# Optimization experiments

Hardware: AMD Instinct MI355X
Metric: run time of the kernel (lower is better)

The kernel has to match this reference:

```python
import jax, jax.numpy as jnp
import numpy as np

N, E = 50000, 1600000
D_IN, D_OUT = 256, 64
ALPHA = 0.2        # LeakyReLU slope used on attention logits (self.leakyrelu)
BT_SLOPE = 0.01    # F.leaky_relu default slope inside relu_bt


def _xavier_normal(key, shape, gain):
    fan_in, fan_out = shape[0], shape[1]
    std = gain * np.sqrt(2.0 / (fan_in + fan_out))
    return jax.random.normal(key, shape, dtype=jnp.float32) * std


def relu_bt(x):
    # -threshold(-leaky_relu(x), -t, -t) == min(leaky_relu(x), t), t = ||x||_inf (detached)
    t = jax.lax.stop_gradient(jnp.max(jnp.abs(x)))
    y = jnp.where(x >= 0, x, BT_SLOPE * x)
    return jnp.minimum(y, t)


def setup_inputs() -> dict:
    key = jax.random.key(0)
    k0, k1, k2, k3, k4, k5 = jax.random.split(key, 6)
    inp = jax.random.normal(k0, (N, D_IN), dtype=jnp.float32)
    edge = jax.random.randint(k1, (2, E), 0, N, dtype=jnp.int64)
    W_high = _xavier_normal(k2, (D_IN, D_OUT), 1.414)
    W_low = _xavier_normal(k3, (D_IN, D_OUT), 1.414)
    a_high = _xavier_normal(k4, (1, D_OUT), 1.414)
    a_low = _xavier_normal(k5, (1, D_OUT), 1.414)
    return {"input": inp, "edge": edge, "W_high": W_high, "W_low": W_low,
            "a_high": a_high, "a_low": a_low}


def reference(input, edge, W_high, W_low, a_high, a_low):
    n = input.shape[0]
    src, dst = edge[0], edge[1]

    h_high = relu_bt(input @ W_high)  # [N, D_OUT]
    h_low = relu_bt(input @ W_low)    # [N, D_OUT]

    # a @ (h[src] -/+ h[dst])^T == (a.h)[src] -/+ (a.h)[dst]: compute per-node scalar
    # projections first, then gather scalars per edge (avoids [E, D_OUT] edge features).
    s_high = h_high @ a_high[0]       # [N]
    s_low = h_low @ a_low[0]          # [N]

    def lrelu(x):
        return jnp.where(x >= 0, x, ALPHA * x)

    edge_e_high = jnp.exp(-lrelu(s_high[src] - s_high[dst]))  # [E]
    edge_e_low = jnp.exp(-lrelu(s_low[src] + s_low[dst]))     # [E]
    # dropout p=0.0 -> identity

    # sparse A @ ones -> per-row sum of attention weights
    rowsum_high = jax.ops.segment_sum(edge_e_high, src, num_segments=n)[:, None]
    rowsum_low = jax.ops.segment_sum(edge_e_low, src, num_segments=n)[:, None]

    # sparse A @ h -> weighted aggregation of neighbor features
    hp_high = jax.ops.segment_sum(edge_e_high[:, None] * h_high[dst], src, num_segments=n)
    hp_low = jax.ops.segment_sum(edge_e_low[:, None] * h_low[dst], src, num_segments=n)

    hp_high = hp_high / (rowsum_high + 1e-16)
    hp_low = hp_low / (rowsum_low + 1e-16)

    # concat=True branch
    return relu_bt(jnp.concatenate([hp_high, hp_low], axis=1))  # [N, 2*D_OUT]
```

## Files before the change

### kernel.cpp

```cpp
#include <hip/hip_runtime.h>
#include <hip/hip_bf16.h>
#include <cstdint>

#define NN    50000
#define NE    1600000
#define DIN   256
#define DOUT  64
#define CAPS  96
#define CAPD  95

#define BKT   196
#define BCAP  10240
#define EPB   4096
#define EPT   16
#define NBIN  391
#define MTB   64
#define NGEMM 782

typedef __attribute__((ext_vector_type(8))) short frag8;
typedef __attribute__((ext_vector_type(4))) float fragc;

union PK { __hip_bfloat162 b2; uint32_t u; };
union CH { frag8 v; uint32_t u[4]; };

__device__ __forceinline__ float leaky01(float x) { return x >= 0.f ? x : 0.01f * x; }

__device__ __forceinline__ uint32_t pk2(float lo, float hi) {
  PK p; p.b2 = __float22bfloat162_rn(make_float2(lo, hi)); return p.u;
}

__device__ __forceinline__ int   bcast_i(int v, int lane) {
  return __builtin_amdgcn_readlane(v, lane);
}
__device__ __forceinline__ float bcast_f(float v, int lane) {
  return __int_as_float(__builtin_amdgcn_readlane(__float_as_int(v), lane));
}

__device__ __forceinline__ float bfH(uint32_t u) { return __uint_as_float(u << 16); }
__device__ __forceinline__ float bfL(uint32_t u) { return __uint_as_float(u & 0xffff0000u); }

__global__ __launch_bounds__(256) void prep_kernel(
    const float* __restrict__ Wh, const float* __restrict__ Wl,
    __hip_bfloat16* __restrict__ Wt, int* __restrict__ cursor)
{
  if (blockIdx.x == 0 && threadIdx.x < BKT) cursor[threadIdx.x] = 0;
  int g = blockIdx.x * 256 + threadIdx.x;
  if (g < 2 * DOUT * DIN) {
    int m = g >> 14, rem = g & 16383;
    int n = rem >> 8, k = rem & 255;
    float v = (m ? Wl : Wh)[k * DOUT + n];
    Wt[g] = __float2bfloat16(v);
  }
}

__global__ __launch_bounds__(256) void fused_kernel(
    const float* __restrict__ inp, const __hip_bfloat16* __restrict__ Wt,
    const float* __restrict__ ah, const float* __restrict__ al,
    const int* __restrict__ edge, int* __restrict__ cursor,
    uint32_t* __restrict__ binned, uint32_t* __restrict__ HL,
    float2* __restrict__ ss)
{
  __shared__ __align__(16) char smem[32768];

  const int idx = blockIdx.x;
  const int t = threadIdx.x;

  if (idx < NBIN) {
    uint32_t* stage  = (uint32_t*)smem;
    int*      hist   = (int*)(smem + 16384);
    int*      cur    = (int*)(smem + 17168);
    int*      base_g = (int*)(smem + 17952);
    int*      scan_s = (int*)(smem + 18736);

    const int e0 = idx * EPB;
    uint32_t v[EPT];
#pragma unroll
    for (int i = 0; i < EPT; i++) {
      int e = e0 + i * 256 + t;
      if (e < NE) {
        uint32_t s = (uint32_t)edge[e];
        uint32_t d = (uint32_t)edge[NE + e];
        v[i] = (s << 16) | d;
      } else {
        v[i] = 0xFFFFFFFFu;
      }
    }
    for (int b = t; b < BKT; b += 256) { hist[b] = 0; cur[b] = 0; }
    __syncthreads();
#pragma unroll
    for (int i = 0; i < EPT; i++) {
      int b = v[i] >> 24;
      if (b < BKT) atomicAdd(&hist[b], 1);
    }
    __syncthreads();
    if (t == 0) {
      int acc = 0;
      for (int b = 0; b < BKT; b++) { scan_s[b] = acc; acc += hist[b]; }
      scan_s[BKT] = acc;
    }
    __syncthreads();
    for (int b = t; b < BKT; b += 256) {
      int h = hist[b];
      base_g[b] = h ? atomicAdd(&cursor[b], h) : 0;
    }
    __syncthreads();
#pragma unroll
    for (int i = 0; i < EPT; i++) {
      int b = v[i] >> 24;
      if (b < BKT) {
        int pos = atomicAdd(&cur[b], 1);
        stage[scan_s[b] + pos] = v[i];
      }
    }
    __syncthreads();
    const int total = scan_s[BKT];
    for (int i = t; i < total; i += 256) {
      int lo = 0, hi = BKT - 1;
      while (lo < hi) { int mid = (lo + hi + 1) >> 1; if (scan_s[mid] <= i) lo = mid; else hi = mid - 1; }
      int ofs = base_g[lo] + (i - scan_s[lo]);
      if (ofs < BCAP) binned[(size_t)lo * BCAP + ofs] = stage[i];
    }
    return;
  }

  frag8* asmem = (frag8*)smem;
  const int gid = idx - NBIN;
  const int n0 = gid * MTB;
  const int lane = t & 63;
  const int w = t >> 6;
  const int quad = lane >> 4, nn = lane & 15;

  const float4* inp4 = (const float4*)inp;
#pragma unroll
  for (int i = 0; i < 8; i++) {
    int c = i * 256 + t;
    int r = c & 15;
    int cc = c >> 4;
    int qd = cc & 3;
    int wq = cc >> 2;
    int row = ((wq >> 3) << 4) + r;
    int k0 = ((wq & 7) << 5) + (qd << 3);
    int node = n0 + row;
    float4 a0 = make_float4(0.f, 0.f, 0.f, 0.f), a1 = a0;
    if (node < NN) {
      a0 = inp4[(size_t)node * 64 + (k0 >> 2)];
      a1 = inp4[(size_t)node * 64 + (k0 >> 2) + 1];
    }
    CH ch;
    ch.u[0] = pk2(a0.x, a0.y);
    ch.u[1] = pk2(a0.z, a0.w);
    ch.u[2] = pk2(a1.x, a1.y);
    ch.u[3] = pk2(a1.z, a1.w);
    asmem[c] = ch.v;
  }
  __syncthreads();

  fragc accH[4], accL[4];
#pragma unroll
  for (int c = 0; c < 4; c++) {
    accH[c] = (fragc){0.f, 0.f, 0.f, 0.f};
    accL[c] = (fragc){0.f, 0.f, 0.f, 0.f};
  }

  const frag8* Wt8 = (const frag8*)Wt;
#pragma unroll
  for (int q = 0; q < 8; q++) {
    frag8 af = asmem[(w << 9) + (q << 6) + lane];
#pragma unroll
    for (int c = 0; c < 4; c++) {
      frag8 bh = Wt8[(c * 16 + nn) * 32 + q * 4 + quad];
      frag8 bl = Wt8[(64 + c * 16 + nn) * 32 + q * 4 + quad];
      accH[c] = __builtin_amdgcn_mfma_f32_16x16x32_bf16(af, bh, accH[c], 0, 0, 0);
      accL[c] = __builtin_amdgcn_mfma_f32_16x16x32_bf16(af, bl, accL[c], 0, 0, 0);
    }
  }

  float ahv[4], alv[4];
#pragma unroll
  for (int c = 0; c < 4; c++) { ahv[c] = ah[c * 16 + nn]; alv[c] = al[c * 16 + nn]; }
#pragma unroll
  for (int r = 0; r < 4; r++) {
    int node = n0 + (w << 4) + (quad << 2) + r;
    float sH = 0.f, sL = 0.f;
#pragma unroll
    for (int c = 0; c < 4; c++) {
      float hH = leaky01(accH[c][r]);
      float hL = leaky01(accL[c][r]);
      if (node < NN) HL[(size_t)node * DOUT + c * 16 + nn] = pk2(hH, hL);
      sH += hH * ahv[c];
      sL += hL * alv[c];
    }
#pragma unroll
    for (int off = 1; off < 16; off <<= 1) {
      sH += __shfl_xor(sH, off);
      sL += __shfl_xor(sL, off);
    }
    if (nn == 0 && node < NN) ss[node] = make_float2(sH, sL);
  }
}

__global__ __launch_bounds__(1024) void csr_kernel(
    const uint32_t* __restrict__ binned, const int* __restrict__ cursor,
    int* __restrict__ col)
{
  __shared__ int cnt[256];
  const int b = blockIdx.x;
  const int t = threadIdx.x;
  if (t < 256) cnt[t] = 0;
  __syncthreads();
  int n = cursor[b]; if (n > BCAP) n = BCAP;
  const uint32_t* eb = binned + (size_t)b * BCAP;
  for (int i = t; i < n; i += 1024) {
    uint32_t v = eb[i];
    int src = v >> 16, dst = v & 0xffff;
    int pos = atomicAdd(&cnt[src & 255], 1);
    if (pos < CAPD) col[(size_t)src * CAPS + 1 + pos] = dst;
  }
  __syncthreads();
  if (t < 256) {
    int node = (b << 8) + t;
    if (node < NN) {
      int c = cnt[t]; if (c > CAPD) c = CAPD;
      col[(size_t)node * CAPS] = c;
    }
  }
}

__global__ __launch_bounds__(256) void agg_kernel(
    const uint32_t* __restrict__ HL, const float2* __restrict__ ss,
    const int* __restrict__ col, float* __restrict__ out)
{
  int wave = (blockIdx.x * blockDim.x + threadIdx.x) >> 6;
  int lane = threadIdx.x & 63;
  if (wave >= NN) return;
  const int n = wave;
  const int* cl = col + (size_t)n * CAPS;
  int d = cl[0]; if (d > CAPD) d = CAPD;

  const float2 sn = ss[n];

  float accH = 0.f, accL = 0.f, rsH = 0.f, rsL = 0.f;

  for (int base = 0; base < d; base += 64) {
    int m = d - base; if (m > 64) m = 64;
    int   dst_l = 0;
    float eh_l = 0.f, el_l = 0.f;
    if (lane < m) {
      dst_l = cl[1 + base + lane];
      float2 sd = ss[dst_l];
      float xh = sn.x - sd.x;
      xh = (xh >= 0.f) ? xh : 0.2f * xh;
      eh_l = __expf(-xh);
      float xl = sn.y + sd.y;
      xl = (xl >= 0.f) ? xl : 0.2f * xl;
      el_l = __expf(-xl);
    }
    int j = 0;
    for (; j + 8 <= m; j += 8) {
      uint32_t u[8]; float eh[8], el[8];
#pragma unroll
      for (int x = 0; x < 8; x++) {
        int dd = bcast_i(dst_l, j + x);
        u[x]  = HL[((uint32_t)dd << 6) + lane];
        eh[x] = bcast_f(eh_l, j + x);
        el[x] = bcast_f(el_l, j + x);
      }
#pragma unroll
      for (int x = 0; x < 8; x++) {
        accH += eh[x] * bfH(u[x]); accL += el[x] * bfL(u[x]);
        rsH += eh[x]; rsL += el[x];
      }
    }
    for (; j < m; j++) {
      int      dst = bcast_i(dst_l, j);
      float    eh  = bcast_f(eh_l, j);
      float    el  = bcast_f(el_l, j);
      uint32_t u   = HL[((uint32_t)dst << 6) + lane];
      accH += eh * bfH(u);
      accL += el * bfL(u);
      rsH += eh;
      rsL += el;
    }
  }

  float oh = accH / (rsH + 1e-16f);
  float ol = accL / (rsL + 1e-16f);
  out[(size_t)n * 128 + lane]      = leaky01(oh);
  out[(size_t)n * 128 + 64 + lane] = leaky01(ol);
}

extern "C" void kernel_launch(void* const* d_in, const int* in_sizes, int n_in,
                              void* d_out, int out_size, void* d_ws, size_t ws_size,
                              hipStream_t stream) {
  const float* inp  = (const float*)d_in[0];
  const int*   edge = (const int*)d_in[1];
  const float* Wh   = (const float*)d_in[2];
  const float* Wl   = (const float*)d_in[3];
  const float* ah   = (const float*)d_in[4];
  const float* al   = (const float*)d_in[5];
  float* out = (float*)d_out;

  char* ws = (char*)d_ws;
  uint32_t* HL     = (uint32_t*)(ws + 0);
  float2*   ss     = (float2*)  (ws + 12800000);
  int*      col    = (int*)     (ws + 13200000);
  uint32_t* binned = (uint32_t*)(ws + 32400000);
  int*      cursor = (int*)     (ws + 40428160);
  __hip_bfloat16* Wt = (__hip_bfloat16*)(ws + 13200000);

  prep_kernel<<<128, 256, 0, stream>>>(Wh, Wl, Wt, cursor);
  fused_kernel<<<NBIN + NGEMM, 256, 0, stream>>>(inp, Wt, ah, al, edge,
                                                 cursor, binned, HL, ss);
  csr_kernel<<<BKT, 1024, 0, stream>>>(binned, cursor, col);
  agg_kernel<<<NN / 4, 256, 0, stream>>>(HL, ss, col, out);
}
```

Before: 218.1 us.

## Build padded adjacency directly with global atomics, drop binning and CSR kernel

Replaces the two-stage bucket sort (shared-memory binning plus a separate csr_kernel) with direct per-edge global atomicAdd on a per-node counter that writes the destination straight into the padded adjacency list, removing one kernel launch and the intermediate binned buffer. The GEMM blocks now keep the whole weight column tile in registers per wave and loop over the four row tiles, with a shared-memory cross-wave reduction for the attention scalars. Global atomics on 1.6M random addresses may contend and are slower per op than shared atomics, and neighbor order becomes nondeterministic.

After: 234.1 us. +7.4%, slower.

```diff
diff --git a/kernel.cpp b/kernel.cpp
--- a/kernel.cpp
+++ b/kernel.cpp
@@ -9,11 +9,8 @@
 #define CAPS  96
 #define CAPD  95
 
-#define BKT   196
-#define BCAP  10240
 #define EPB   4096
-#define EPT   16
-#define NBIN  391
+#define NBLD  391
 #define MTB   64
 #define NGEMM 782
 
@@ -41,10 +38,10 @@
 
 __global__ __launch_bounds__(256) void prep_kernel(
     const float* __restrict__ Wh, const float* __restrict__ Wl,
-    __hip_bfloat16* __restrict__ Wt, int* __restrict__ cursor)
+    __hip_bfloat16* __restrict__ Wt, int* __restrict__ ncnt)
 {
-  if (blockIdx.x == 0 && threadIdx.x < BKT) cursor[threadIdx.x] = 0;
   int g = blockIdx.x * 256 + threadIdx.x;
+  if (g < NN) ncnt[g] = 0;
   if (g < 2 * DOUT * DIN) {
     int m = g >> 14, rem = g & 16383;
     int n = rem >> 8, k = rem & 255;
@@ -56,79 +53,44 @@
 __global__ __launch_bounds__(256) void fused_kernel(
     const float* __restrict__ inp, const __hip_bfloat16* __restrict__ Wt,
     const float* __restrict__ ah, const float* __restrict__ al,
-    const int* __restrict__ edge, int* __restrict__ cursor,
-    uint32_t* __restrict__ binned, uint32_t* __restrict__ HL,
-    float2* __restrict__ ss)
+    const int* __restrict__ edge, int* __restrict__ ncnt,
+    int* __restrict__ col, uint32_t* __restrict__ HL, float2* __restrict__ ss)
 {
   __shared__ __align__(16) char smem[32768];
 
   const int idx = blockIdx.x;
   const int t = threadIdx.x;
 
-  if (idx < NBIN) {
-    uint32_t* stage  = (uint32_t*)smem;
-    int*      hist   = (int*)(smem + 16384);
-    int*      cur    = (int*)(smem + 17168);
-    int*      base_g = (int*)(smem + 17952);
-    int*      scan_s = (int*)(smem + 18736);
-
+  if (idx < NBLD) {
     const int e0 = idx * EPB;
-    uint32_t v[EPT];
-#pragma unroll
-    for (int i = 0; i < EPT; i++) {
+#pragma unroll
+    for (int i = 0; i < 16; i++) {
       int e = e0 + i * 256 + t;
       if (e < NE) {
-        uint32_t s = (uint32_t)edge[e];
-        uint32_t d = (uint32_t)edge[NE + e];
-        v[i] = (s << 16) | d;
-      } else {
-        v[i] = 0xFFFFFFFFu;
-      }
-    }
-    for (int b = t; b < BKT; b += 256) { hist[b] = 0; cur[b] = 0; }
-    __syncthreads();
-#pragma unroll
-    for (int i = 0; i < EPT; i++) {
-      int b = v[i] >> 24;
-      if (b < BKT) atomicAdd(&hist[b], 1);
-    }
-    __syncthreads();
-    if (t == 0) {
-      int acc = 0;
-      for (int b = 0; b < BKT; b++) { scan_s[b] = acc; acc += hist[b]; }
-      scan_s[BKT] = acc;
-    }
-    __syncthreads();
-    for (int b = t; b < BKT; b += 256) {
-      int h = hist[b];
-      base_g[b] = h ? atomicAdd(&cursor[b], h) : 0;
-    }
-    __syncthreads();
-#pragma unroll
-    for (int i = 0; i < EPT; i++) {
-      int b = v[i] >> 24;
-      if (b < BKT) {
-        int pos = atomicAdd(&cur[b], 1);
-        stage[scan_s[b] + pos] = v[i];
-      }
-    }
-    __syncthreads();
-    const int total = scan_s[BKT];
-    for (int i = t; i < total; i += 256) {
-      int lo = 0, hi = BKT - 1;
-      while (lo < hi) { int mid = (lo + hi + 1) >> 1; if (scan_s[mid] <= i) lo = mid; else hi = mid - 1; }
-      int ofs = base_g[lo] + (i - scan_s[lo]);
-      if (ofs < BCAP) binned[(size_t)lo * BCAP + ofs] = stage[i];
+        int s = edge[e];
+        int d = edge[NE + e];
+        int pos = atomicAdd(&ncnt[s], 1);
+        if (pos < CAPD) col[(size_t)s * CAPS + 1 + pos] = d;
+      }
     }
     return;
   }
 
   frag8* asmem = (frag8*)smem;
-  const int gid = idx - NBIN;
+  const int gid = idx - NBLD;
   const int n0 = gid * MTB;
   const int lane = t & 63;
   const int w = t >> 6;
   const int quad = lane >> 4, nn = lane & 15;
+
+  const frag8* Wt8 = (const frag8*)Wt;
+  const int bbase = ((w * 16 + nn) << 5) + quad;
+  frag8 bH[8], bL[8];
+#pragma unroll
+  for (int q = 0; q < 8; q++) {
+    bH[q] = Wt8[bbase + (q << 2)];
+    bL[q] = Wt8[2048 + bbase + (q << 2)];
+  }
 
   const float4* inp4 = (const float4*)inp;
 #pragma unroll
@@ -157,85 +119,68 @@
 
   fragc accH[4], accL[4];
 #pragma unroll
-  for (int c = 0; c < 4; c++) {
-    accH[c] = (fragc){0.f, 0.f, 0.f, 0.f};
-    accL[c] = (fragc){0.f, 0.f, 0.f, 0.f};
-  }
-
-  const frag8* Wt8 = (const frag8*)Wt;
+  for (int m = 0; m < 4; m++) {
+    accH[m] = (fragc){0.f, 0.f, 0.f, 0.f};
+    accL[m] = (fragc){0.f, 0.f, 0.f, 0.f};
+  }
+
 #pragma unroll
   for (int q = 0; q < 8; q++) {
-    frag8 af = asmem[(w << 9) + (q << 6) + lane];
-#pragma unroll
-    for (int c = 0; c < 4; c++) {
-      frag8 bh = Wt8[(c * 16 + nn) * 32 + q * 4 + quad];
-      frag8 bl = Wt8[(64 + c * 16 + nn) * 32 + q * 4 + quad];
-      accH[c] = __builtin_amdgcn_mfma_f32_16x16x32_bf16(af, bh, accH[c], 0, 0, 0);
-      accL[c] = __builtin_amdgcn_mfma_f32_16x16x32_bf16(af, bl, accL[c], 0, 0, 0);
-    }
-  }
-
-  float ahv[4], alv[4];
-#pragma unroll
-  for (int c = 0; c < 4; c++) { ahv[c] = ah[c * 16 + nn]; alv[c] = al[c * 16 + nn]; }
-#pragma unroll
-  for (int r = 0; r < 4; r++) {
-    int node = n0 + (w << 4) + (quad << 2) + r;
-    float sH = 0.f, sL = 0.f;
-#pragma unroll
-    for (int c = 0; c < 4; c++) {
-      float hH = leaky01(accH[c][r]);
-      float hL = leaky01(accL[c][r]);
-      if (node < NN) HL[(size_t)node * DOUT + c * 16 + nn] = pk2(hH, hL);
-      sH += hH * ahv[c];
-      sL += hL * alv[c];
-    }
-#pragma unroll
-    for (int off = 1; off < 16; off <<= 1) {
-      sH += __shfl_xor(sH, off);
-      sL += __shfl_xor(sL, off);
-    }
-    if (nn == 0 && node < NN) ss[node] = make_float2(sH, sL);
-  }
-}
-
-__global__ __launch_bounds__(1024) void csr_kernel(
-    const uint32_t* __restrict__ binned, const int* __restrict__ cursor,
-    int* __restrict__ col)
-{
-  __shared__ int cnt[256];
-  const int b = blockIdx.x;
-  const int t = threadIdx.x;
-  if (t < 256) cnt[t] = 0;
+#pragma unroll
+    for (int mt = 0; mt < 4; mt++) {
+      frag8 af = asmem[(mt << 9) + (q << 6) + lane];
+      accH[mt] = __builtin_amdgcn_mfma_f32_16x16x32_bf16(af, bH[q], accH[mt], 0, 0, 0);
+      accL[mt] = __builtin_amdgcn_mfma_f32_16x16x32_bf16(af, bL[q], accL[mt], 0, 0, 0);
+    }
+  }
   __syncthreads();
-  int n = cursor[b]; if (n > BCAP) n = BCAP;
-  const uint32_t* eb = binned + (size_t)b * BCAP;
-  for (int i = t; i < n; i += 1024) {
-    uint32_t v = eb[i];
-    int src = v >> 16, dst = v & 0xffff;
-    int pos = atomicAdd(&cnt[src & 255], 1);
-    if (pos < CAPD) col[(size_t)src * CAPS + 1 + pos] = dst;
+
+  float* sred = (float*)smem;
+  const float ahv = ah[w * 16 + nn];
+  const float alv = al[w * 16 + nn];
+#pragma unroll
+  for (int mt = 0; mt < 4; mt++) {
+#pragma unroll
+    for (int r = 0; r < 4; r++) {
+      int rowb = (mt << 4) + (quad << 2) + r;
+      int node = n0 + rowb;
+      float hH = leaky01(accH[mt][r]);
+      float hL = leaky01(accL[mt][r]);
+      if (node < NN) HL[(size_t)node * DOUT + w * 16 + nn] = pk2(hH, hL);
+      float pH = hH * ahv, pL = hL * alv;
+#pragma unroll
+      for (int off = 1; off < 16; off <<= 1) {
+        pH += __shfl_xor(pH, off);
+        pL += __shfl_xor(pL, off);
+      }
+      if (nn == 0) {
+        sred[rowb * 8 + w]     = pH;
+        sred[rowb * 8 + 4 + w] = pL;
+      }
+    }
   }
   __syncthreads();
-  if (t < 256) {
-    int node = (b << 8) + t;
+  if (t < 64) {
+    int node = n0 + t;
     if (node < NN) {
-      int c = cnt[t]; if (c > CAPD) c = CAPD;
-      col[(size_t)node * CAPS] = c;
+      float sH = sred[t * 8 + 0] + sred[t * 8 + 1] + sred[t * 8 + 2] + sred[t * 8 + 3];
+      float sL = sred[t * 8 + 4] + sred[t * 8 + 5] + sred[t * 8 + 6] + sred[t * 8 + 7];
+      ss[node] = make_float2(sH, sL);
     }
   }
 }
 
 __global__ __launch_bounds__(256) void agg_kernel(
     const uint32_t* __restrict__ HL, const float2* __restrict__ ss,
-    const int* __restrict__ col, float* __restrict__ out)
+    const int* __restrict__ col, const int* __restrict__ ncnt,
+    float* __restrict__ out)
 {
   int wave = (blockIdx.x * blockDim.x + threadIdx.x) >> 6;
   int lane = threadIdx.x & 63;
   if (wave >= NN) return;
   const int n = wave;
   const int* cl = col + (size_t)n * CAPS;
-  int d = cl[0]; if (d > CAPD) d = CAPD;
+  int d = ncnt[n]; if (d > CAPD) d = CAPD;
 
   const float2 sn = ss[n];
 
@@ -301,16 +246,14 @@
   float* out = (float*)d_out;
 
   char* ws = (char*)d_ws;
-  uint32_t* HL     = (uint32_t*)(ws + 0);
-  float2*   ss     = (float2*)  (ws + 12800000);
-  int*      col    = (int*)     (ws + 13200000);
-  uint32_t* binned = (uint32_t*)(ws + 32400000);
-  int*      cursor = (int*)     (ws + 40428160);
-  __hip_bfloat16* Wt = (__hip_bfloat16*)(ws + 13200000);
-
-  prep_kernel<<<128, 256, 0, stream>>>(Wh, Wl, Wt, cursor);
-  fused_kernel<<<NBIN + NGEMM, 256, 0, stream>>>(inp, Wt, ah, al, edge,
-                                                 cursor, binned, HL, ss);
-  csr_kernel<<<BKT, 1024, 0, stream>>>(binned, cursor, col);
-  agg_kernel<<<NN / 4, 256, 0, stream>>>(HL, ss, col, out);
-}
+  uint32_t* HL   = (uint32_t*)(ws + 0);
+  float2*   ss   = (float2*)  (ws + 12800000);
+  int*      col  = (int*)     (ws + 13200000);
+  __hip_bfloat16* Wt = (__hip_bfloat16*)(ws + 32400000);
+  int*      ncnt = (int*)     (ws + 32500000);
+
+  prep_kernel<<<196, 256, 0, stream>>>(Wh, Wl, Wt, ncnt);
+  fused_kernel<<<NBLD + NGEMM, 256, 0, stream>>>(inp, Wt, ah, al, edge,
+                                                 ncnt, col, HL, ss);
+  agg_kernel<<<NN / 4, 256, 0, stream>>>(HL, ss, col, ncnt, out);
+}
```

## Partition GEMM waves by output columns and keep W fragments in registers

Applied to the files above, without the earlier changes.

The GEMM tile now gives each wave one 16-column slice of the output, covering all four 16-row tiles, instead of one row tile across all columns. Each wave loads its W fragments into registers once, and A fragments are read from shared memory per row tile, which removes the repeated global loads of W inside the MFMA loop. The per-node attention projection now needs a cross-wave reduction through shared memory, adding two barriers and extra LDS traffic. Holding 16 B fragments raises register pressure.

After: 197.2 us. 9.6% less time.

```diff
diff --git a/kernel.cpp b/kernel.cpp
--- a/kernel.cpp
+++ b/kernel.cpp
@@ -129,6 +129,15 @@
   const int lane = t & 63;
   const int w = t >> 6;
   const int quad = lane >> 4, nn = lane & 15;
+
+  const frag8* Wt8 = (const frag8*)Wt;
+  const int bbase = ((w * 16 + nn) << 5) + quad;
+  frag8 bH[8], bL[8];
+#pragma unroll
+  for (int q = 0; q < 8; q++) {
+    bH[q] = Wt8[bbase + (q << 2)];
+    bL[q] = Wt8[2048 + bbase + (q << 2)];
+  }
 
   const float4* inp4 = (const float4*)inp;
 #pragma unroll
@@ -157,45 +166,54 @@
 
   fragc accH[4], accL[4];
 #pragma unroll
-  for (int c = 0; c < 4; c++) {
-    accH[c] = (fragc){0.f, 0.f, 0.f, 0.f};
-    accL[c] = (fragc){0.f, 0.f, 0.f, 0.f};
-  }
-
-  const frag8* Wt8 = (const frag8*)Wt;
+  for (int m = 0; m < 4; m++) {
+    accH[m] = (fragc){0.f, 0.f, 0.f, 0.f};
+    accL[m] = (fragc){0.f, 0.f, 0.f, 0.f};
+  }
+
 #pragma unroll
   for (int q = 0; q < 8; q++) {
-    frag8 af = asmem[(w << 9) + (q << 6) + lane];
-#pragma unroll
-    for (int c = 0; c < 4; c++) {
-      frag8 bh = Wt8[(c * 16 + nn) * 32 + q * 4 + quad];
-      frag8 bl = Wt8[(64 + c * 16 + nn) * 32 + q * 4 + quad];
-      accH[c] = __builtin_amdgcn_mfma_f32_16x16x32_bf16(af, bh, accH[c], 0, 0, 0);
-      accL[c] = __builtin_amdgcn_mfma_f32_16x16x32_bf16(af, bl, accL[c], 0, 0, 0);
-    }
-  }
-
-  float ahv[4], alv[4];
-#pragma unroll
-  for (int c = 0; c < 4; c++) { ahv[c] = ah[c * 16 + nn]; alv[c] = al[c * 16 + nn]; }
-#pragma unroll
-  for (int r = 0; r < 4; r++) {
-    int node = n0 + (w << 4) + (quad << 2) + r;
-    float sH = 0.f, sL = 0.f;
-#pragma unroll
-    for (int c = 0; c < 4; c++) {
-      float hH = leaky01(accH[c][r]);
-      float hL = leaky01(accL[c][r]);
-      if (node < NN) HL[(size_t)node * DOUT + c * 16 + nn] = pk2(hH, hL);
-      sH += hH * ahv[c];
-      sL += hL * alv[c];
-    }
-#pragma unroll
-    for (int off = 1; off < 16; off <<= 1) {
-      sH += __shfl_xor(sH, off);
-      sL += __shfl_xor(sL, off);
-    }
-    if (nn == 0 && node < NN) ss[node] = make_float2(sH, sL);
+#pragma unroll
+    for (int mt = 0; mt < 4; mt++) {
+      frag8 af = asmem[(mt << 9) + (q << 6) + lane];
+      accH[mt] = __builtin_amdgcn_mfma_f32_16x16x32_bf16(af, bH[q], accH[mt], 0, 0, 0);
+      accL[mt] = __builtin_amdgcn_mfma_f32_16x16x32_bf16(af, bL[q], accL[mt], 0, 0, 0);
+    }
+  }
+  __syncthreads();
+
+  float* sred = (float*)smem;
+  const float ahv = ah[w * 16 + nn];
+  const float alv = al[w * 16 + nn];
+#pragma unroll
+  for (int mt = 0; mt < 4; mt++) {
+#pragma unroll
+    for (int r = 0; r < 4; r++) {
+      int rowb = (mt << 4) + (quad << 2) + r;
+      int node = n0 + rowb;
+      float hH = leaky01(accH[mt][r]);
+      float hL = leaky01(accL[mt][r]);
+      if (node < NN) HL[(size_t)node * DOUT + w * 16 + nn] = pk2(hH, hL);
+      float pH = hH * ahv, pL = hL * alv;
+#pragma unroll
+      for (int off = 1; off < 16; off <<= 1) {
+        pH += __shfl_xor(pH, off);
+        pL += __shfl_xor(pL, off);
+      }
+      if (nn == 0) {
+        sred[rowb * 8 + w]     = pH;
+        sred[rowb * 8 + 4 + w] = pL;
+      }
+    }
+  }
+  __syncthreads();
+  if (t < 64) {
+    int node = n0 + t;
+    if (node < NN) {
+      float sH = sred[t * 8 + 0] + sred[t * 8 + 1] + sred[t * 8 + 2] + sred[t * 8 + 3];
+      float sL = sred[t * 8 + 4] + sred[t * 8 + 5] + sred[t * 8 + 6] + sred[t * 8 + 7];
+      ss[node] = make_float2(sH, sL);
+    }
   }
 }
 
```
